# Kernel optimization log

Measured on AMD Instinct MI355X. Metric: run time of the kernel, lower is better.

The kernel has to match this reference:

```python
import jax, jax.numpy as jnp
import numpy as np

D_MODEL = 2048
D_LATENT = 512


def setup_inputs() -> dict:
    key = jax.random.key(0)
    ks = jax.random.split(key, 6)
    x = jax.random.normal(ks[0], (2, 4096, D_MODEL), dtype=jnp.float32)
    cache = jax.random.normal(ks[1], (2, 4096, D_LATENT), dtype=jnp.float32)
    s = 0.02
    # weights stored (in_features, out_features); equivalent to torch Linear (no bias)
    W_kv = jax.random.normal(ks[2], (D_MODEL, D_LATENT), dtype=jnp.float32) * s
    W_q = jax.random.normal(ks[3], (D_MODEL, D_MODEL), dtype=jnp.float32) * s
    W_lq = jax.random.normal(ks[4], (D_MODEL, D_LATENT), dtype=jnp.float32) * s
    W_o = jax.random.normal(ks[5], (D_LATENT, D_MODEL), dtype=jnp.float32) * s
    return {"x": x, "cache": cache, "W_kv": W_kv, "W_q": W_q, "W_lq": W_lq, "W_o": W_o}


def reference(x, cache, W_kv, W_q, W_lq, W_o):
    # latent compression of inputs: (B, S, d_latent)
    l_kv_new = jnp.einsum('bsd,dl->bsl', x, W_kv)
    # query path: x -> query (d_model) -> latent query (d_latent)
    q = jnp.einsum('bsd,de->bse', x, W_q)
    lq = jnp.einsum('bse,el->bsl', q, W_lq)
    # append to cache: (B, T+S, d_latent)
    l_kv = jnp.concatenate([cache, l_kv_new], axis=1)
    scale = jnp.sqrt(jnp.float32(D_LATENT)).astype(x.dtype)
    # attention in latent space: scores (B, S, T+S)
    scores = jnp.einsum('bsl,btl->bst', lq, l_kv) / scale
    weights = jax.nn.softmax(scores, axis=-1)
    ctx = jnp.einsum('bst,btl->bsl', weights, l_kv)
    out = jnp.einsum('bsl,ld->bsd', ctx, W_o)
    return out, l_kv
```

## Files before the change

kernel.cpp:

```cpp
#include <hip/hip_runtime.h>
#include <hip/hip_bf16.h>
#include <math.h>


typedef _Float16 f16x8 __attribute__((ext_vector_type(8)));
typedef _Float16 f16x4 __attribute__((ext_vector_type(4)));
typedef float    f32x4 __attribute__((ext_vector_type(4)));
typedef float    f32x8 __attribute__((ext_vector_type(8)));

__device__ __forceinline__ void gl_lds16(const void* g, void* l) {
  __builtin_amdgcn_global_load_lds(
      (const __attribute__((address_space(1))) void*)g,
      (__attribute__((address_space(3))) void*)l, 16, 0, 0);
}


__global__ __launch_bounds__(256) void k_cvt(const float* __restrict__ in,
                                             _Float16* __restrict__ out, int n4) {
  int i = blockIdx.x * blockDim.x + threadIdx.x;
  int st = gridDim.x * blockDim.x;
  for (; i < n4; i += st) {
    f32x4 v = reinterpret_cast<const f32x4*>(in)[i];
    reinterpret_cast<f16x4*>(out)[i] = __builtin_convertvector(v, f16x4);
  }
}

__global__ __launch_bounds__(256) void k_cache(const float* __restrict__ cache,
                                               float* __restrict__ lkv_f32,
                                               _Float16* __restrict__ lkv16, int n4) {
  int i = blockIdx.x * blockDim.x + threadIdx.x;
  int st = gridDim.x * blockDim.x;
  for (; i < n4; i += st) {
    f32x4 v = reinterpret_cast<const f32x4*>(cache)[i];
    int e = i << 2;
    int b = e >> 21;
    int dst = e + (b << 21);
    *reinterpret_cast<f32x4*>(lkv_f32 + dst) = v;
    *reinterpret_cast<f16x4*>(lkv16 + dst) = __builtin_convertvector(v, f16x4);
  }
}

__global__ __launch_bounds__(256) void k_tc(const float* __restrict__ in,
                                            _Float16* __restrict__ out, int R, int C) {
  __shared__ float t[32][33];
  const int c0 = blockIdx.x << 5, r0 = blockIdx.y << 5;
  const int tid = threadIdx.x;
  {
    int r = tid >> 3, c4 = (tid & 7) << 2;
    f32x4 v = *reinterpret_cast<const f32x4*>(&in[(long)(r0 + r) * C + c0 + c4]);
    t[r][c4] = v[0]; t[r][c4 + 1] = v[1]; t[r][c4 + 2] = v[2]; t[r][c4 + 3] = v[3];
  }
  __syncthreads();
  {
    int c = tid >> 3, r4 = (tid & 7) << 2;
    f16x4 o = {(_Float16)t[r4][c], (_Float16)t[r4 + 1][c],
               (_Float16)t[r4 + 2][c], (_Float16)t[r4 + 3][c]};
    *reinterpret_cast<f16x4*>(&out[(long)(c0 + c) * R + r0 + r4]) = o;
  }
}

__global__ __launch_bounds__(256) void k_tb(const _Float16* __restrict__ in,
                                            _Float16* __restrict__ out, int R, int C) {
  __shared__ _Float16 t[32][36];
  const int c0 = blockIdx.x << 5, r0 = blockIdx.y << 5;
  const int tid = threadIdx.x;
  {
    int r = tid >> 3, c4 = (tid & 7) << 2;
    f16x4 v = *reinterpret_cast<const f16x4*>(&in[(long)(r0 + r) * C + c0 + c4]);
    t[r][c4] = v[0]; t[r][c4 + 1] = v[1]; t[r][c4 + 2] = v[2]; t[r][c4 + 3] = v[3];
  }
  __syncthreads();
  {
    int c = tid >> 3, r4 = (tid & 7) << 2;
    f16x4 o = {t[r4][c], t[r4 + 1][c], t[r4 + 2][c], t[r4 + 3][c]};
    *reinterpret_cast<f16x4*>(&out[(long)(c0 + c) * R + r0 + r4]) = o;
  }
}

template <int CMODE, int AF32, int BF32, int SWZ>
__global__ __launch_bounds__(256) void k_gemm(const void* __restrict__ Av,
                                              const void* __restrict__ Bv,
                                              float* __restrict__ Cf,
                                              _Float16* __restrict__ Ch,
                                              _Float16* __restrict__ Ch2,
                                              int M, int N, int K, int lda, int ldb,
                                              float cscale) {
  const _Float16* A16 = (const _Float16*)Av;
  const float*    A32 = (const float*)Av;
  const _Float16* B16 = (const _Float16*)Bv;
  const float*    B32 = (const float*)Bv;
  if constexpr (CMODE == 4) {
    const long z = blockIdx.z;
    A16 += z * K; A32 += z * K;
    B16 += z * K; B32 += z * K;
    Cf += z * (long)M * N;
  }
  int bxr = blockIdx.x, byr = blockIdx.y;
  if constexpr (SWZ) {
    const int nbx = gridDim.x, nby = gridDim.y, nwg = nbx * nby;
    if ((nwg & 7) == 0) {
      const int orig = bxr * nby + byr;
      const int q = nwg >> 3;
      const int wg = (orig & 7) * q + (orig >> 3);
      bxr = wg / nby; byr = wg % nby;
    }
  }
  __shared__ alignas(16) _Float16 As[128 * 64];
  __shared__ alignas(16) _Float16 Bs[128 * 64];
  const int tid = threadIdx.x;
  const int lane = tid & 63;
  const int w = tid >> 6;
  const int wr = ((w >> 1) & 1) << 6, wc = (w & 1) << 6;
  const int bm = bxr << 7, bn = byr << 7;
  const int g = lane >> 4, ln15 = lane & 15;

  f32x4 acc[4][4] = {};

  const int srowl = lane >> 3;
  const int skcol = (lane & 7) << 3;
  const int wofs = (srowl << 6) + (((lane & 7) ^ srowl) << 3);

  f16x8 ra[4], rb[4];
  auto loadregs = [&](int k0) {
#pragma unroll
    for (int i = 0; i < 4; ++i) {
      int ch = (w << 2) + i;
      int row = (ch << 3) + srowl;
      if constexpr (AF32) {
        f32x8 v = *reinterpret_cast<const f32x8*>(&A32[(long)(bm + row) * lda + k0 + skcol]);
        ra[i] = __builtin_convertvector(v, f16x8);
      } else {
        ra[i] = *reinterpret_cast<const f16x8*>(&A16[(long)(bm + row) * lda + k0 + skcol]);
      }
      if constexpr (BF32) {
        f32x8 v = *reinterpret_cast<const f32x8*>(&B32[(long)(bn + row) * ldb + k0 + skcol]);
        rb[i] = __builtin_convertvector(v, f16x8);
      } else {
        rb[i] = *reinterpret_cast<const f16x8*>(&B16[(long)(bn + row) * ldb + k0 + skcol]);
      }
    }
  };
  loadregs(0);
  const int nk = K >> 6;
  for (int kt = 0; kt < nk; ++kt) {
    __syncthreads();
#pragma unroll
    for (int i = 0; i < 4; ++i) {
      int ch = (w << 2) + i;
      *reinterpret_cast<f16x8*>(&As[(ch << 9) + wofs]) = ra[i];
      *reinterpret_cast<f16x8*>(&Bs[(ch << 9) + wofs]) = rb[i];
    }
    __syncthreads();
    if (kt + 1 < nk) loadregs((kt + 1) << 6);
#pragma unroll
    for (int ks = 0; ks < 2; ++ks) {
      f16x8 af[4], bf[4];
#pragma unroll
      for (int i = 0; i < 4; ++i) {
        const int arow = wr + (i << 4) + ln15;
        const int brow = wc + (i << 4) + ln15;
        const int inner = (((ks << 5) + (g << 3)) ^ ((ln15 & 7) << 3));
        af[i] = *reinterpret_cast<const f16x8*>(&As[arow * 64 + inner]);
        bf[i] = *reinterpret_cast<const f16x8*>(&Bs[brow * 64 + inner]);
      }
#pragma unroll
      for (int i = 0; i < 4; ++i)
#pragma unroll
        for (int j = 0; j < 4; ++j)
          acc[i][j] = __builtin_amdgcn_mfma_f32_16x16x32_f16(af[i], bf[j], acc[i][j], 0, 0, 0);
    }
  }
#pragma unroll
  for (int i = 0; i < 4; ++i) {
    const int row = bm + wr + (i << 4) + (g << 2);
#pragma unroll
    for (int j = 0; j < 4; ++j) {
      const int col = bn + wc + (j << 4) + ln15;
#pragma unroll
      for (int r = 0; r < 4; ++r) {
        float v = acc[i][j][r];
        long orow = row + r;
        if constexpr (CMODE == 1) {
          Ch[orow * N + col] = (_Float16)v;
        } else if constexpr (CMODE == 3) {
          Ch[orow * N + col] = (_Float16)(v * cscale);
        } else if constexpr (CMODE == 5) {
          if (col < 512) {
            Ch[orow * 512 + col] = (_Float16)v;
          } else {
            long m2 = ((orow >> 12) << 13) + 4096 + (orow & 4095);
            Cf[m2 * 512 + (col - 512)] = v;
            Ch2[m2 * 512 + (col - 512)] = (_Float16)v;
          }
        } else {
          Cf[orow * N + col] = v;
        }
      }
    }
  }
}

template <int CMODE, int STATS, int SPLITK>
__global__ __launch_bounds__(512, 2) void k_gemm256(const _Float16* __restrict__ A,
                                                    const _Float16* __restrict__ B,
                                                    float* __restrict__ Cf,
                                                    _Float16* __restrict__ Ch,
                                                    float* __restrict__ Lp,
                                                    int M, int N, int K,
                                                    int lda, int ldb) {
  extern __shared__ _Float16 sm[];
  _Float16* As = sm;
  _Float16* Bs = sm + 32768;
  if constexpr (SPLITK) {
    const long z = blockIdx.z;
    A += z * (long)K;
    B += z * (long)K;
    Ch += z * (long)M * N;
  }
  int bxr = blockIdx.x, byr = blockIdx.y;
  {
    const int nbx = gridDim.x, nby = gridDim.y, nwg = nbx * nby;
    if ((nwg & 7) == 0) {
      const int orig = bxr * nby + byr;
      const int q = nwg >> 3;
      const int wg = (orig & 7) * q + (orig >> 3);
      bxr = wg / nby; byr = wg % nby;
    }
  }
  const int tid = threadIdx.x;
  const int lane = tid & 63;
  const int w = tid >> 6;
  const int wm = w >> 2, wn = w & 3;
  const int bm = bxr << 8, bn = byr << 8;
  const int g = lane >> 4, ln15 = lane & 15;

  f32x4 acc[8][4] = {};

  const int lrow8 = lane >> 3;
  const int lswz  = ((lane & 7) ^ lrow8) << 3;
  const _Float16* Ap[4];
  const _Float16* Bp[4];
  int loff[4];
#pragma unroll
  for (int i = 0; i < 4; ++i) {
    const int row = (i << 6) + (w << 3) + lrow8;
    Ap[i] = &A[(long)(bm + row) * lda + lswz];
    Bp[i] = &B[(long)(bn + row) * ldb + lswz];
    loff[i] = ((i << 6) + (w << 3)) << 6;
  }

  auto stage = [&](int buf, int kt) {
    const int k0 = kt << 6;
    const int bo = buf << 14;
#pragma unroll
    for (int i = 0; i < 4; ++i) {
      gl_lds16(Ap[i] + k0, &As[bo + loff[i]]);
      gl_lds16(Bp[i] + k0, &Bs[bo + loff[i]]);
    }
  };

  const int nk = K >> 6;
  stage(0, 0);
  if (nk > 1) stage(1, 1);

  for (int kt = 0; kt < nk; ++kt) {
    if (kt + 1 < nk) asm volatile("s_waitcnt vmcnt(8)" ::: "memory");
    else             asm volatile("s_waitcnt vmcnt(0)" ::: "memory");
    __builtin_amdgcn_sched_barrier(0);
    __builtin_amdgcn_s_barrier();
    const int bo = (kt & 1) << 14;
#pragma unroll
    for (int ks = 0; ks < 2; ++ks) {
      f16x8 af[8], bf[4];
      const int innersw = ((ks << 5) + (g << 3)) ^ ((ln15 & 7) << 3);
#pragma unroll
      for (int i = 0; i < 8; ++i) {
        const int arow = (wm << 7) + (i << 4) + ln15;
        af[i] = *reinterpret_cast<const f16x8*>(&As[bo + arow * 64 + innersw]);
      }
#pragma unroll
      for (int j = 0; j < 4; ++j) {
        const int brow = (wn << 6) + (j << 4) + ln15;
        bf[j] = *reinterpret_cast<const f16x8*>(&Bs[bo + brow * 64 + innersw]);
      }
      __builtin_amdgcn_s_setprio(1);
#pragma unroll
      for (int i = 0; i < 8; ++i)
#pragma unroll
        for (int j = 0; j < 4; ++j)
          acc[i][j] = __builtin_amdgcn_mfma_f32_16x16x32_f16(af[i], bf[j], acc[i][j], 0, 0, 0);
      __builtin_amdgcn_s_setprio(0);
    }
    asm volatile("s_waitcnt lgkmcnt(0)" ::: "memory");
    __builtin_amdgcn_sched_barrier(0);
    __builtin_amdgcn_s_barrier();
    if (kt + 2 < nk) stage(kt & 1, kt + 2);
  }

  if constexpr (STATS) {
    float* Lsh = (float*)sm;
    float part[8][4];
#pragma unroll
    for (int i = 0; i < 8; ++i) {
      const int row = bm + (wm << 7) + (i << 4) + (g << 2);
#pragma unroll
      for (int r = 0; r < 4; ++r) {
        float s = 0.f;
#pragma unroll
        for (int j = 0; j < 4; ++j) {
          const int col = bn + (wn << 6) + (j << 4) + ln15;
          float e = fminf(__expf(acc[i][j][r]), 60000.f);
          Ch[(long)(row + r) * N + col] = (_Float16)e;
          s += e;
        }
#pragma unroll
        for (int off = 1; off < 16; off <<= 1) s += __shfl_xor(s, off);
        part[i][r] = s;
      }
    }
    if (ln15 == 0) {
#pragma unroll
      for (int i = 0; i < 8; ++i)
#pragma unroll
        for (int r = 0; r < 4; ++r) {
          const int lrow = (wm << 7) + (i << 4) + (g << 2) + r;
          Lsh[(lrow << 2) + wn] = part[i][r];
        }
    }
    __syncthreads();
    if (tid < 256) {
      float L = Lsh[(tid << 2)] + Lsh[(tid << 2) + 1] +
                Lsh[(tid << 2) + 2] + Lsh[(tid << 2) + 3];
      Lp[(long)(bm + tid) * gridDim.y + byr] = L;
    }
  } else {
#pragma unroll
    for (int i = 0; i < 8; ++i) {
      const int row = bm + (wm << 7) + (i << 4) + (g << 2);
#pragma unroll
      for (int j = 0; j < 4; ++j) {
        const int col = bn + (wn << 6) + (j << 4) + ln15;
#pragma unroll
        for (int r = 0; r < 4; ++r) {
          if constexpr (CMODE == 1)
            Ch[(long)(row + r) * N + col] = (_Float16)acc[i][j][r];
          else
            Cf[(long)(row + r) * N + col] = acc[i][j][r];
        }
      }
    }
  }
}

__global__ __launch_bounds__(256) void k_linv(const float* __restrict__ Lp,
                                              float* __restrict__ Linv, int nb) {
  const int r = (blockIdx.x << 8) + threadIdx.x;
  float s = 0.f;
  for (int i = 0; i < nb; ++i) s += Lp[(long)r * nb + i];
  Linv[r] = 1.f / s;
}

__global__ __launch_bounds__(256) void k_red4(const float* __restrict__ p,
                                              _Float16* __restrict__ o,
                                              int n4, float scale) {
  const f32x4* pv = reinterpret_cast<const f32x4*>(p);
  int i = blockIdx.x * blockDim.x + threadIdx.x;
  int st = gridDim.x * blockDim.x;
  for (; i < n4; i += st) {
    f32x4 a = pv[i] + pv[i + n4] + pv[i + 2 * n4] + pv[i + 3 * n4];
    a *= scale;
    reinterpret_cast<f16x4*>(o)[i] = __builtin_convertvector(a, f16x4);
  }
}

__global__ __launch_bounds__(256) void k_red8row(const _Float16* __restrict__ p,
                                                 const float* __restrict__ Linv,
                                                 _Float16* __restrict__ o, int n4) {
  const f16x4* pv = reinterpret_cast<const f16x4*>(p);
  int i = blockIdx.x * blockDim.x + threadIdx.x;
  int st = gridDim.x * blockDim.x;
  for (; i < n4; i += st) {
    f32x4 a = __builtin_convertvector(pv[i], f32x4);
#pragma unroll
    for (int s = 1; s < 8; ++s)
      a += __builtin_convertvector(pv[i + (long)s * n4], f32x4);
    a *= Linv[i >> 7];
    reinterpret_cast<f16x4*>(o)[i] = __builtin_convertvector(a, f16x4);
  }
}


extern "C" void kernel_launch(void* const* d_in, const int* in_sizes, int n_in,
                              void* d_out, int out_size, void* d_ws, size_t ws_size,
                              hipStream_t stream) {
  const float* x     = (const float*)d_in[0];
  const float* cache = (const float*)d_in[1];
  const float* W_kv  = (const float*)d_in[2];
  const float* W_q   = (const float*)d_in[3];
  const float* W_lq  = (const float*)d_in[4];
  const float* W_o   = (const float*)d_in[5];

  float* out     = (float*)d_out;
  float* lkv_out = out + (size_t)8192 * 2048;

  _Float16* base16 = (_Float16*)d_out;
  _Float16* x16    = base16;
  _Float16* lq16   = base16 + 16777216;
  _Float16* WlqT   = base16 + 25165824;
  _Float16* WcombT = base16 + 26214400;
  _Float16* WkvT   = base16 + 27262976;
  _Float16* lkvT16 = base16 + 20971520;
  _Float16* PVp16  = base16;
  float*    Lp     = (float*)(base16 + 29360128);
  float*    Linv   = Lp + 131072;

  _Float16* lkv16 = (_Float16*)d_ws;
  _Float16* ctx   = lkv16 + 8388608;
  _Float16* WoT   = ctx + 4194304;
  _Float16* Sbuf  = WoT + 1048576;
  float*    Wcp   = (float*)Sbuf;

  const size_t sbase = 27262976;
  int CR = 1024;
  if (ws_size >= sbase + (size_t)4096 * 8192 * 2) CR = 4096;
  else if (ws_size >= sbase + (size_t)2048 * 8192 * 2) CR = 2048;

  const float iscale = 0.044194173824159216f;

  hipFuncSetAttribute((const void*)k_gemm256<1, 1, 0>,
                      hipFuncAttributeMaxDynamicSharedMemorySize, 131072);
  hipFuncSetAttribute((const void*)k_gemm256<0, 0, 0>,
                      hipFuncAttributeMaxDynamicSharedMemorySize, 131072);
  hipFuncSetAttribute((const void*)k_gemm256<1, 0, 1>,
                      hipFuncAttributeMaxDynamicSharedMemorySize, 131072);

  k_cvt<<<1024, 256, 0, stream>>>(x, x16, 16777216 / 4);
  k_cache<<<1024, 256, 0, stream>>>(cache, lkv_out, lkv16, 4194304 / 4);
  k_tc<<<dim3(16, 64), 256, 0, stream>>>(W_kv, WkvT, 2048, 512);
  k_tc<<<dim3(16, 64), 256, 0, stream>>>(W_lq, WlqT, 2048, 512);
  k_tc<<<dim3(64, 16), 256, 0, stream>>>(W_o, WoT, 512, 2048);

  k_gemm<4, 0, 1, 0><<<dim3(4, 16, 4), 256, 0, stream>>>(
      WlqT, W_q, Wcp, nullptr, nullptr, 512, 2048, 512, 2048, 2048, 1.f);
  k_red4<<<1024, 256, 0, stream>>>(Wcp, WcombT, (512 * 2048) / 4, iscale);
  k_gemm<5, 0, 0, 1><<<dim3(64, 8), 256, 0, stream>>>(
      x16, WcombT, lkv_out, lq16, lkv16, 8192, 1024, 2048, 2048, 2048, 1.f);
  k_tb<<<dim3(16, 512), 256, 0, stream>>>(lkv16, lkvT16, 16384, 512);

  for (long r0 = 0; r0 < 8192; r0 += CR) {
    const long b = r0 >> 12;
    k_gemm256<1, 1, 0><<<dim3(CR >> 8, 32), 512, 131072, stream>>>(
        lq16 + r0 * 512, lkv16 + b * 8192 * 512, nullptr, Sbuf, Lp,
        CR, 8192, 512, 512, 512);
    k_linv<<<CR >> 8, 256, 0, stream>>>(Lp, Linv, 32);
    k_gemm256<1, 0, 1><<<dim3(CR >> 8, 2, 8), 512, 131072, stream>>>(
        Sbuf, lkvT16 + b * 8192, nullptr, PVp16, nullptr,
        CR, 512, 1024, 8192, 16384);
    k_red8row<<<2048, 256, 0, stream>>>(PVp16, Linv, ctx + r0 * 512, (CR * 512) / 4);
  }

  k_gemm256<0, 0, 0><<<dim3(32, 8), 512, 131072, stream>>>(ctx, WoT, out, nullptr,
                                                           nullptr,
                                                           8192, 2048, 512, 512, 512);
}
```

Measured before the change: 339.2 us.

## Split GEMM main loop into four phases interleaving half-tile prefetch with MFMA

Restructures the 256x256 fp16 GEMM main loop so A and B tiles are staged as separate half-tiles into four LDS slots. Each k-step is split into four phases, and each phase issues one half-tile global->LDS load for the next A or next-next B tile before running its share of MFMAs. The intent is to spread memory traffic across the compute and replace the bulk stage-after-barrier pattern with finer-grained overlap. This costs more barriers per k-step and relies on careful vmcnt accounting, which could serialize waves or race if the counts are wrong.

```diff
diff --git a/kernel.cpp b/kernel.cpp
--- a/kernel.cpp
+++ b/kernel.cpp
@@ -238,63 +238,88 @@
 
   const int lrow8 = lane >> 3;
   const int lswz  = ((lane & 7) ^ lrow8) << 3;
-  const _Float16* Ap[4];
-  const _Float16* Bp[4];
-  int loff[4];
-#pragma unroll
-  for (int i = 0; i < 4; ++i) {
-    const int row = (i << 6) + (w << 3) + lrow8;
-    Ap[i] = &A[(long)(bm + row) * lda + lswz];
-    Bp[i] = &B[(long)(bn + row) * ldb + lswz];
-    loff[i] = ((i << 6) + (w << 3)) << 6;
-  }
-
-  auto stage = [&](int buf, int kt) {
-    const int k0 = kt << 6;
-    const int bo = buf << 14;
-#pragma unroll
-    for (int i = 0; i < 4; ++i) {
-      gl_lds16(Ap[i] + k0, &As[bo + loff[i]]);
-      gl_lds16(Bp[i] + k0, &Bs[bo + loff[i]]);
+  const int nk = K >> 6;
+
+  auto stageA = [&](int half, int kt) {
+    const int slot = ((kt & 1) << 1) + half;
+    const long k0 = (long)kt << 6;
+#pragma unroll
+    for (int l = 0; l < 2; ++l) {
+      const int row = (half << 7) + (l << 6) + (w << 3) + lrow8;
+      gl_lds16(&A[(long)(bm + row) * lda + k0 + lswz],
+               &As[slot * 8192 + (((l << 6) + (w << 3)) << 6)]);
     }
   };
-
-  const int nk = K >> 6;
-  stage(0, 0);
-  if (nk > 1) stage(1, 1);
-
+  auto stageB = [&](int half, int kt) {
+    const int slot = ((kt & 1) << 1) + half;
+    const long k0 = (long)kt << 6;
+#pragma unroll
+    for (int l = 0; l < 2; ++l) {
+      const int row = (half << 7) + (l << 6) + (w << 3) + lrow8;
+      gl_lds16(&B[(long)(bn + row) * ldb + k0 + lswz],
+               &Bs[slot * 8192 + (((l << 6) + (w << 3)) << 6)]);
+    }
+  };
+
+  stageB(0, 0); stageB(1, 0);
+  stageA(0, 0); stageA(1, 0);
+  if (nk > 1) { stageB(0, 1); stageB(1, 1); }
+  if (nk > 1) asm volatile("s_waitcnt vmcnt(4)" ::: "memory");
+  else        asm volatile("s_waitcnt vmcnt(0)" ::: "memory");
+  __builtin_amdgcn_sched_barrier(0);
+  __builtin_amdgcn_s_barrier();
+
+  f16x8 bf[4][2];
   for (int kt = 0; kt < nk; ++kt) {
-    if (kt + 1 < nk) asm volatile("s_waitcnt vmcnt(8)" ::: "memory");
-    else             asm volatile("s_waitcnt vmcnt(0)" ::: "memory");
-    __builtin_amdgcn_sched_barrier(0);
-    __builtin_amdgcn_s_barrier();
-    const int bo = (kt & 1) << 14;
-#pragma unroll
-    for (int ks = 0; ks < 2; ++ks) {
-      f16x8 af[8], bf[4];
-      const int innersw = ((ks << 5) + (g << 3)) ^ ((ln15 & 7) << 3);
-#pragma unroll
-      for (int i = 0; i < 8; ++i) {
-        const int arow = (wm << 7) + (i << 4) + ln15;
-        af[i] = *reinterpret_cast<const f16x8*>(&As[bo + arow * 64 + innersw]);
-      }
-#pragma unroll
-      for (int j = 0; j < 4; ++j) {
-        const int brow = (wn << 6) + (j << 4) + ln15;
-        bf[j] = *reinterpret_cast<const f16x8*>(&Bs[bo + brow * 64 + innersw]);
-      }
+    const int aslot = ((kt & 1) << 1) + wm;
+    const int bslot = ((kt & 1) << 1) + (wn >> 1);
+    const int brow0 = (wn & 1) << 6;
+#pragma unroll
+    for (int p = 0; p < 4; ++p) {
+      if (p == 0) {
+#pragma unroll
+        for (int j = 0; j < 4; ++j)
+#pragma unroll
+          for (int ks = 0; ks < 2; ++ks) {
+            const int inner = ((ks << 5) + (g << 3)) ^ ((ln15 & 7) << 3);
+            bf[j][ks] = *reinterpret_cast<const f16x8*>(
+                &Bs[bslot * 8192 + (brow0 + (j << 4) + ln15) * 64 + inner]);
+          }
+      }
+      f16x8 af[2][2];
+#pragma unroll
+      for (int i = 0; i < 2; ++i)
+#pragma unroll
+        for (int ks = 0; ks < 2; ++ks) {
+          const int mf = (p << 1) + i;
+          const int inner = ((ks << 5) + (g << 3)) ^ ((ln15 & 7) << 3);
+          af[i][ks] = *reinterpret_cast<const f16x8*>(
+              &As[aslot * 8192 + ((mf << 4) + ln15) * 64 + inner]);
+        }
+      if (p == 0 && kt + 1 < nk) stageA(0, kt + 1);
+      if (p == 1 && kt + 1 < nk) stageA(1, kt + 1);
+      if (p == 2 && kt + 2 < nk) stageB(0, kt + 2);
+      if (p == 3 && kt + 2 < nk) stageB(1, kt + 2);
+      __builtin_amdgcn_s_barrier();
+      asm volatile("s_waitcnt lgkmcnt(0)" ::: "memory");
+      __builtin_amdgcn_sched_barrier(0);
       __builtin_amdgcn_s_setprio(1);
 #pragma unroll
-      for (int i = 0; i < 8; ++i)
+      for (int i = 0; i < 2; ++i)
 #pragma unroll
         for (int j = 0; j < 4; ++j)
-          acc[i][j] = __builtin_amdgcn_mfma_f32_16x16x32_f16(af[i], bf[j], acc[i][j], 0, 0, 0);
+#pragma unroll
+          for (int ks = 0; ks < 2; ++ks)
+            acc[(p << 1) + i][j] = __builtin_amdgcn_mfma_f32_16x16x32_f16(
+                af[i][ks], bf[j][ks], acc[(p << 1) + i][j], 0, 0, 0);
       __builtin_amdgcn_s_setprio(0);
-    }
-    asm volatile("s_waitcnt lgkmcnt(0)" ::: "memory");
-    __builtin_amdgcn_sched_barrier(0);
-    __builtin_amdgcn_s_barrier();
-    if (kt + 2 < nk) stage(kt & 1, kt + 2);
+      if (p == 3) {
+        if (kt + 2 < nk) asm volatile("s_waitcnt vmcnt(4)" ::: "memory");
+        else             asm volatile("s_waitcnt vmcnt(0)" ::: "memory");
+        __builtin_amdgcn_sched_barrier(0);
+      }
+      __builtin_amdgcn_s_barrier();
+    }
   }
 
   if constexpr (STATS) {
```

Measured after the change: 332.6 us. No clear change (-2.0%).
